# Kernel tuning notes

Measured on AMD Instinct MI355X. Metric: run time of the kernel, lower is better.

The kernel has to match this reference:

```python
import jax, jax.numpy as jnp
import numpy as np

B, S, D, H, M = 2, 2048, 1024, 16, 4096  # batch, seqlen, dim, n_heads, max_seq_len
HD = D // H  # head_dim = 64
EPS = 1e-5


def layernorm(x, g, b):
    mu = jnp.mean(x, axis=-1, keepdims=True)
    var = jnp.mean((x - mu) ** 2, axis=-1, keepdims=True)
    return (x - mu) * jax.lax.rsqrt(var + EPS) * g + b


def setup_inputs() -> dict:
    key = jax.random.key(0)
    ks = jax.random.split(key, 5)
    x = jax.random.normal(ks[0], (B, S, D), jnp.float32)
    # causal mask: >=0 -> keep, negative -> drop (forward does att *= mask >= 0)
    i = jnp.arange(S)
    mask = jnp.where(i[None, :] <= i[:, None], 0, -1).astype(jnp.int32)[None, None]
    w1 = jax.random.normal(ks[1], (4 * D, D), jnp.float32) * (D ** -0.5)
    b1 = jnp.zeros((4 * D,), jnp.float32)
    w2 = jax.random.normal(ks[2], (D, D), jnp.float32) * (D ** -0.5)
    b2 = jnp.zeros((D,), jnp.float32)
    g1 = jnp.ones((D,), jnp.float32)
    beta1 = jnp.zeros((D,), jnp.float32)
    g2 = jnp.ones((D,), jnp.float32)
    beta2 = jnp.zeros((D,), jnp.float32)
    pos_w = jax.random.normal(ks[3], (2 * M - 1,), jnp.float32) * 0.02
    return dict(x=x, mask=mask, w1=w1, b1=b1, w2=w2, b2=b2,
                g1=g1, beta1=beta1, g2=g2, beta2=beta2, pos_w=pos_w)


def reference(x, mask, w1, b1, w2, b2, g1, beta1, g2, beta2, pos_w):
    # f1 + silu, split into gate u and q/k/v
    h = jax.nn.silu(x @ w1.T + b1)                      # [B,S,4D]
    u, q, k, v = jnp.split(h, 4, axis=-1)
    to_heads = lambda t: t.reshape(B, S, H, HD).transpose(0, 2, 1, 3)  # [B,H,S,HD]
    u, q, k, v = map(to_heads, (u, q, k, v))
    # relative positional bias: bias[i,j] = pos_w[M-1 + (j - i)]
    rel = jnp.arange(S)[None, :] - jnp.arange(S)[:, None]
    bias = pos_w[M - 1 + rel]                           # [S,S]
    att = jax.nn.silu(jnp.einsum('bhqd,bhkd->bhqk', q, k) + bias)
    att = att * (mask >= 0)                             # [B,H,S,S]
    y = jnp.einsum('bhqk,bhkd->bhqd', att, v) * u
    y = y.transpose(0, 2, 1, 3).reshape(B, S, D)
    y = layernorm(y, g1, beta1)
    y = y @ w2.T + b2
    return layernorm(y + x, g2, beta2)
```

## Files before the change

kernel.cpp:

```cpp
#include <hip/hip_runtime.h>
#include <hip/hip_bf16.h>

#define BN   2
#define SEQ  2048
#define DIM  1024
#define NH   16
#define HD   64
#define D4   4096
#define MAXS 4096

using bf16 = __hip_bfloat16;
typedef __bf16 bf16x8 __attribute__((ext_vector_type(8)));
typedef float  f32x4  __attribute__((ext_vector_type(4)));

__device__ __forceinline__ float bf2f(bf16 v){ return __bfloat162float(v); }
__device__ __forceinline__ bf16  f2bf(float v){ return __float2bfloat16(v); }
__device__ __forceinline__ float silu_f(float v){
  const float e = __expf(-v);
  return v * __builtin_amdgcn_rcpf(1.f + e);
}

__device__ __forceinline__ void async16(void* lds, const void* g){
  __builtin_amdgcn_global_load_lds((const __attribute__((address_space(1))) void*)g,
                                   (__attribute__((address_space(3))) void*)lds, 16, 0, 0);
}
__device__ __forceinline__ f32x4 mfma16(bf16x8 a, bf16x8 b, f32x4 c){
  return __builtin_amdgcn_mfma_f32_16x16x32_bf16(a, b, c, 0, 0, 0);
}

__global__ __launch_bounds__(256) void f2bk3(
    const float* __restrict__ a, bf16* __restrict__ ao, int na,
    const float* __restrict__ b, bf16* __restrict__ bo, int nb,
    const float* __restrict__ c, bf16* __restrict__ co)
{
  int i = (blockIdx.x * 256 + threadIdx.x) * 4;
  const float* in; bf16* out;
  if (i < na){ in = a; out = ao; }
  else if (i < na + nb){ in = b; out = bo; i -= na; }
  else { in = c; out = co; i -= na + nb; }
  const float4 v = *(const float4*)(in + i);
  bf16 t0 = f2bf(v.x), t1 = f2bf(v.y), t2 = f2bf(v.z), t3 = f2bf(v.w);
  ushort4 o;
  o.x = *(unsigned short*)&t0; o.y = *(unsigned short*)&t1;
  o.z = *(unsigned short*)&t2; o.w = *(unsigned short*)&t3;
  *(ushort4*)((unsigned short*)out + i) = o;
}

template<int NTOT>
__global__ __launch_bounds__(256) void gemm_bt(
    const bf16* __restrict__ A, const bf16* __restrict__ W,
    const float* __restrict__ bias, bf16* __restrict__ outb, bf16* __restrict__ vt)
{
  constexpr int K = DIM;
  const int ntiles = NTOT / 128;
  const int m0 = (int)(blockIdx.x / ntiles) * 128;
  const int n0 = (int)(blockIdx.x % ntiles) * 128;
  __shared__ bf16 Al[2*128*32];
  __shared__ bf16 Bl[2*128*32];
  const int tid = threadIdx.x, wave = tid>>6, lane = tid&63;
  const int quad = lane>>4, l16 = lane&15;
  const int srow = lane>>2;
  const int sg   = ((lane&3) ^ ((lane>>3)&3)) * 8;
  const int wm = (wave>>1)*64, wn = (wave&1)*64;
  const int rkey = ((l16>>1)&3);

  f32x4 acc[4][4];
  #pragma unroll
  for (int i=0;i<4;i++)
    #pragma unroll
    for (int j=0;j<4;j++) acc[i][j] = (f32x4){0.f,0.f,0.f,0.f};

  const bf16* aB = A + m0*K;
  const bf16* wB = W + n0*K;

  for (int k0 = 0; k0 < K; k0 += 64){
    #pragma unroll
    for (int s=0;s<2;s++){
      const int kc = k0 + s*32;
      async16(&Al[s*4096 + wave*1024      ], aB + (wave*32      + srow)*K + kc + sg);
      async16(&Al[s*4096 + wave*1024 + 512], aB + (wave*32 + 16 + srow)*K + kc + sg);
      async16(&Bl[s*4096 + wave*1024      ], wB + (wave*32      + srow)*K + kc + sg);
      async16(&Bl[s*4096 + wave*1024 + 512], wB + (wave*32 + 16 + srow)*K + kc + sg);
    }
    __syncthreads();
    #pragma unroll
    for (int s=0;s<2;s++){
      bf16x8 af[4], bv[4];
      #pragma unroll
      for (int mt=0;mt<4;mt++) af[mt] = *(const bf16x8*)&Al[s*4096 + (wm+mt*16+l16)*32 + (quad ^ rkey)*8];
      #pragma unroll
      for (int nt=0;nt<4;nt++) bv[nt] = *(const bf16x8*)&Bl[s*4096 + (wn+nt*16+l16)*32 + (quad ^ rkey)*8];
      #pragma unroll
      for (int mt=0;mt<4;mt++)
        #pragma unroll
        for (int nt=0;nt<4;nt++)
          acc[mt][nt] = mfma16(af[mt], bv[nt], acc[mt][nt]);
    }
    __syncthreads();
  }

  const bool vtile = (NTOT == 4096) && (n0 >= 3*DIM);
  if (!vtile){
    #pragma unroll
    for (int mt=0;mt<4;mt++){
      #pragma unroll
      for (int nt=0;nt<4;nt++){
        const int row = m0 + wm + mt*16 + quad*4;
        const int col = n0 + wn + nt*16 + l16;
        const float bvv = bias[col];
        #pragma unroll
        for (int r=0;r<4;r++){
          float v = silu_f(acc[mt][nt][r] + bvv);
          outb[(row+r)*NTOT + col] = f2bf(v);
        }
      }
    }
  } else {
    #pragma unroll
    for (int mt=0;mt<4;mt++){
      #pragma unroll
      for (int nt=0;nt<4;nt++){
        const int row = m0 + wm + mt*16 + quad*4;
        const int colg = n0 + wn + nt*16 + l16;
        const float bvv = bias[colg];
        const int col = colg - 3*DIM;
        const int hh = col >> 6, d = col & 63;
        const int bb = row >> 11, sl = row & 2047;
        ushort4 o;
        float v0 = silu_f(acc[mt][nt][0] + bvv);
        float v1 = silu_f(acc[mt][nt][1] + bvv);
        float v2 = silu_f(acc[mt][nt][2] + bvv);
        float v3 = silu_f(acc[mt][nt][3] + bvv);
        bf16 t0=f2bf(v0), t1=f2bf(v1), t2=f2bf(v2), t3=f2bf(v3);
        o.x=*(unsigned short*)&t0; o.y=*(unsigned short*)&t1;
        o.z=*(unsigned short*)&t2; o.w=*(unsigned short*)&t3;
        *(ushort4*)&vt[((bb*NH + hh)*HD + d)*SEQ + sl] = o;
      }
    }
  }
}

__global__ __launch_bounds__(256) void gemm_bt2(
    const bf16* __restrict__ A, const bf16* __restrict__ W,
    const float* __restrict__ bias, const float* __restrict__ resid,
    float* __restrict__ outf)
{
  constexpr int K = DIM, NTOT = DIM;
  const int ntiles = NTOT / 64;
  const int m0 = (int)(blockIdx.x / ntiles) * 128;
  const int n0 = (int)(blockIdx.x % ntiles) * 64;
  __shared__ bf16 Al[2*128*32];
  __shared__ bf16 Bl[2*64*32];
  const int tid = threadIdx.x, wave = tid>>6, lane = tid&63;
  const int quad = lane>>4, l16 = lane&15;
  const int srow = lane>>2;
  const int sg   = ((lane&3) ^ ((lane>>3)&3)) * 8;
  const int wm = wave*32;
  const int rkey = ((l16>>1)&3);

  f32x4 acc[2][4];
  #pragma unroll
  for (int i=0;i<2;i++)
    #pragma unroll
    for (int j=0;j<4;j++) acc[i][j] = (f32x4){0.f,0.f,0.f,0.f};

  const bf16* aB = A + m0*K;
  const bf16* wB = W + n0*K;

  for (int k0 = 0; k0 < K; k0 += 64){
    #pragma unroll
    for (int s=0;s<2;s++){
      const int kc = k0 + s*32;
      async16(&Al[s*4096 + wave*1024      ], aB + (wave*32      + srow)*K + kc + sg);
      async16(&Al[s*4096 + wave*1024 + 512], aB + (wave*32 + 16 + srow)*K + kc + sg);
      async16(&Bl[s*2048 + wave*512       ], wB + (wave*16      + srow)*K + kc + sg);
    }
    __syncthreads();
    #pragma unroll
    for (int s=0;s<2;s++){
      bf16x8 af[2], bv[4];
      #pragma unroll
      for (int mt=0;mt<2;mt++) af[mt] = *(const bf16x8*)&Al[s*4096 + (wm+mt*16+l16)*32 + (quad ^ rkey)*8];
      #pragma unroll
      for (int nt=0;nt<4;nt++) bv[nt] = *(const bf16x8*)&Bl[s*2048 + (nt*16+l16)*32 + (quad ^ rkey)*8];
      #pragma unroll
      for (int mt=0;mt<2;mt++)
        #pragma unroll
        for (int nt=0;nt<4;nt++)
          acc[mt][nt] = mfma16(af[mt], bv[nt], acc[mt][nt]);
    }
    __syncthreads();
  }

  #pragma unroll
  for (int mt=0;mt<2;mt++){
    #pragma unroll
    for (int nt=0;nt<4;nt++){
      const int row = m0 + wm + mt*16 + quad*4;
      const int col = n0 + nt*16 + l16;
      const float bvv = bias[col];
      #pragma unroll
      for (int r=0;r<4;r++){
        outf[(row+r)*NTOT + col] = acc[mt][nt][r] + bvv + resid[(row+r)*NTOT + col];
      }
    }
  }
}

__global__ __launch_bounds__(256) void attn(
    const bf16* __restrict__ h, const bf16* __restrict__ vt,
    const float* __restrict__ pw, bf16* __restrict__ y)
{
  const int bid = blockIdx.x;
  const int g  = bid & 31;
  const int qt = 31 - (bid >> 5);
  const int hh = g & 15, b = g >> 4;

  __shared__ __align__(16) char smem[16384 + 16384 + 17408 + 1024];
  bf16*  Kl  = (bf16*)smem;
  bf16*  Vl  = (bf16*)(smem + 16384);
  bf16*  Pl  = (bf16*)(smem + 32768);
  float* pwl = (float*)(smem + 50176);

  const int tid = threadIdx.x, wave = tid>>6, lane = tid&63;
  const int quad = lane>>4, l16 = lane&15;

  const bf16* kgb = h + b*SEQ*D4 + 2*DIM + hh*HD;
  const bf16* vgb = vt + (b*NH + hh)*HD*SEQ;
  const int krow8 = lane>>3;
  const int kgo   = ((lane&7) ^ krow8) * 8;
  const int vrow4 = lane>>4;

  const int q0 = qt * 64;

  const bf16* qbase = h + (b*SEQ + q0 + wave*16 + l16)*D4 + DIM + hh*HD;
  bf16x8 qf[2];
  qf[0] = *(const bf16x8*)(qbase + quad*8);
  qf[1] = *(const bf16x8*)(qbase + 32 + quad*8);

  f32x4 oacc[4];
  #pragma unroll
  for (int nt=0;nt<4;nt++) oacc[nt] = (f32x4){0.f,0.f,0.f,0.f};

  const int kmax = q0 + 64;

  bf16x8 kreg[4], vreg[4];
  float pv;
  #pragma unroll
  for (int t=0;t<4;t++)
    kreg[t] = *(const bf16x8*)(kgb + (wave*32 + t*8 + krow8)*D4 + kgo);
  #pragma unroll
  for (int t=0;t<4;t++){
    const int vg = ((lane&15) ^ (t*4 + vrow4)) * 8;
    vreg[t] = *(const bf16x8*)(vgb + (wave*16 + t*4 + vrow4)*SEQ + vg);
  }
  pv = pw[MAXS - 1 - q0 - 63 + tid];

  for (int k0 = 0; k0 < kmax; k0 += 128){
    __syncthreads();
    #pragma unroll
    for (int t=0;t<4;t++)
      *(bf16x8*)&Kl[(wave*32 + t*8)*64 + lane*8] = kreg[t];
    #pragma unroll
    for (int t=0;t<4;t++)
      *(bf16x8*)&Vl[(wave*16 + t*4)*128 + lane*8] = vreg[t];
    pwl[tid] = pv;
    __syncthreads();

    if (k0 + 128 < kmax){
      const int kn = k0 + 128;
      #pragma unroll
      for (int t=0;t<4;t++)
        kreg[t] = *(const bf16x8*)(kgb + (kn + wave*32 + t*8 + krow8)*D4 + kgo);
      #pragma unroll
      for (int t=0;t<4;t++){
        const int vg = ((lane&15) ^ (t*4 + vrow4)) * 8;
        vreg[t] = *(const bf16x8*)(vgb + (wave*16 + t*4 + vrow4)*SEQ + kn + vg);
      }
      pv = pw[MAXS - 1 + kn - q0 - 63 + tid];
    }

    f32x4 sacc[8];
    #pragma unroll
    for (int nt=0;nt<8;nt++) sacc[nt] = (f32x4){0.f,0.f,0.f,0.f};
    __builtin_amdgcn_s_setprio(1);
    #pragma unroll
    for (int ks=0;ks<2;ks++){
      #pragma unroll
      for (int nt=0;nt<8;nt++){
        bf16x8 kf = *(const bf16x8*)&Kl[(nt*16 + l16)*64 + ((ks*4 + quad) ^ (l16&7))*8];
        sacc[nt] = mfma16(kf, qf[ks], sacc[nt]);
      }
    }
    __builtin_amdgcn_s_setprio(0);

    bf16* Plw = Pl + wave*(16*136);
    const int dq = q0 - k0;
    const int qrl = wave*16 + l16;
    if (dq >= 127){
      #pragma unroll
      for (int nt=0;nt<8;nt++){
        const int kb = nt*16 + quad*4;
        ushort4 o; bf16 tb[4];
        #pragma unroll
        for (int r=0;r<4;r++){
          const int d = kb + r - qrl;
          const float bias = pwl[d + 63];
          tb[r] = f2bf(silu_f(sacc[nt][r] + bias));
        }
        o.x=*(unsigned short*)&tb[0]; o.y=*(unsigned short*)&tb[1];
        o.z=*(unsigned short*)&tb[2]; o.w=*(unsigned short*)&tb[3];
        *(ushort4*)&Plw[l16*136 + kb] = o;
      }
    } else {
      #pragma unroll
      for (int nt=0;nt<8;nt++){
        const int kb = nt*16 + quad*4;
        ushort4 o; bf16 tb[4];
        #pragma unroll
        for (int r=0;r<4;r++){
          const int d = kb + r - qrl;
          const float bias = pwl[d + 63];
          const float sv = silu_f(sacc[nt][r] + bias);
          tb[r] = f2bf((d <= dq) ? sv : 0.f);
        }
        o.x=*(unsigned short*)&tb[0]; o.y=*(unsigned short*)&tb[1];
        o.z=*(unsigned short*)&tb[2]; o.w=*(unsigned short*)&tb[3];
        *(ushort4*)&Plw[l16*136 + kb] = o;
      }
    }

    __builtin_amdgcn_s_setprio(1);
    #pragma unroll
    for (int ks=0;ks<4;ks++){
      bf16x8 pf = *(const bf16x8*)&Plw[l16*136 + ks*32 + quad*8];
      #pragma unroll
      for (int nt=0;nt<4;nt++){
        bf16x8 vf = *(const bf16x8*)&Vl[(nt*16 + l16)*128 + ((ks*4 + quad) ^ l16)*8];
        oacc[nt] = mfma16(pf, vf, oacc[nt]);
      }
    }
    __builtin_amdgcn_s_setprio(0);
  }

  const int qrow = q0 + wave*16 + quad*4;
  #pragma unroll
  for (int nt=0;nt<4;nt++){
    const int c = hh*HD + nt*16 + l16;
    #pragma unroll
    for (int r=0;r<4;r++){
      const int srow = b*SEQ + qrow + r;
      const float uu = bf2f(h[srow*D4 + c]);
      y[srow*DIM + c] = f2bf(oacc[nt][r] * uu);
    }
  }
}


template<bool FP32IN, bool FP32OUT>
__global__ __launch_bounds__(256) void lnorm(const void* __restrict__ in,
    const float* __restrict__ g, const float* __restrict__ be, void* __restrict__ out)
{
  const int row = blockIdx.x;
  const int tid = threadIdx.x, wave = tid>>6, lane = tid&63;
  const int c0 = tid*4;
  float v[4];
  if (FP32IN){
    const float* p = (const float*)in + row*DIM + c0;
    #pragma unroll
    for (int j=0;j<4;j++) v[j] = p[j];
  } else {
    const bf16* p = (const bf16*)in + row*DIM + c0;
    #pragma unroll
    for (int j=0;j<4;j++) v[j] = bf2f(p[j]);
  }
  float s = 0.f, ss = 0.f;
  #pragma unroll
  for (int j=0;j<4;j++){ s += v[j]; ss += v[j]*v[j]; }
  #pragma unroll
  for (int off=32; off>0; off>>=1){
    s  += __shfl_down(s, off);
    ss += __shfl_down(ss, off);
  }
  __shared__ float red[8];
  if (lane==0){ red[wave] = s; red[4+wave] = ss; }
  __syncthreads();
  s  = red[0]+red[1]+red[2]+red[3];
  ss = red[4]+red[5]+red[6]+red[7];
  const float mu   = s * (1.f/DIM);
  const float var  = ss * (1.f/DIM) - mu*mu;
  const float rstd = rsqrtf(var + 1e-5f);
  #pragma unroll
  for (int j=0;j<4;j++){
    const int c = c0 + j;
    const float o = (v[j]-mu)*rstd*g[c] + be[c];
    if (FP32OUT) ((float*)out)[row*DIM + c] = o;
    else         ((bf16*)out)[row*DIM + c] = f2bf(o);
  }
}

extern "C" void kernel_launch(void* const* d_in, const int* in_sizes, int n_in,
                              void* d_out, int out_size, void* d_ws, size_t ws_size,
                              hipStream_t stream)
{
  const float* x   = (const float*)d_in[0];
  const float* w1  = (const float*)d_in[2];
  const float* b1  = (const float*)d_in[3];
  const float* w2  = (const float*)d_in[4];
  const float* b2  = (const float*)d_in[5];
  const float* g1  = (const float*)d_in[6];
  const float* be1 = (const float*)d_in[7];
  const float* g2  = (const float*)d_in[8];
  const float* be2 = (const float*)d_in[9];
  const float* pw  = (const float*)d_in[10];

  char* ws = (char*)d_ws;
  bf16*  h   = (bf16*)(ws);
  bf16*  vt  = (bf16*)(ws + (32u<<20));
  bf16*  y   = (bf16*)(ws + (40u<<20));
  bf16*  xb  = (bf16*)(ws + (48u<<20));
  bf16*  w1b = (bf16*)(ws + (56u<<20));
  bf16*  w2b = (bf16*)(ws + (64u<<20));
  bf16*  l1  = (bf16*)(ws + (66u<<20));
  float* z   = (float*)(ws + (74u<<20));

  const int NX  = BN*SEQ*DIM;
  const int NW1 = 4*DIM*DIM;
  const int NW2 = DIM*DIM;
  f2bk3<<<dim3((NX+NW1+NW2)/1024), dim3(256), 0, stream>>>(x, xb, NX, w1, w1b, NW1, w2, w2b);

  gemm_bt<4096><<<dim3(1024), dim3(256), 0, stream>>>(xb, w1b, b1, h, vt);
  attn<<<dim3(1024), dim3(256), 0, stream>>>(h, vt, pw, y);
  lnorm<false,false><<<dim3(4096), dim3(256), 0, stream>>>(y, g1, be1, l1);
  gemm_bt2<<<dim3(512), dim3(256), 0, stream>>>(l1, w2b, b2, x, z);
  lnorm<true,true><<<dim3(4096), dim3(256), 0, stream>>>(z, g2, be2, d_out);
}
```

Before: 236.0 us.

## Double-buffer LDS prefetch in both GEMM kernels to overlap loads with MFMA

Both bf16 GEMM kernels now load the first K=32 slice up front. Each loop iteration then issues async global-to-LDS loads for the next slice into the other buffer before running MFMAs on the current one. Before, each iteration loaded two slices, waited at a barrier and only then computed. The goal is to hide global load latency behind matrix math; the barrier count stays the same but each iteration does less work per barrier.

```diff
diff --git a/kernel.cpp b/kernel.cpp
--- a/kernel.cpp
+++ b/kernel.cpp
@@ -52,6 +52,7 @@
     const float* __restrict__ bias, bf16* __restrict__ outb, bf16* __restrict__ vt)
 {
   constexpr int K = DIM;
+  constexpr int NIT = K / 32;
   const int ntiles = NTOT / 128;
   const int m0 = (int)(blockIdx.x / ntiles) * 128;
   const int n0 = (int)(blockIdx.x % ntiles) * 128;
@@ -73,23 +74,31 @@
   const bf16* aB = A + m0*K;
   const bf16* wB = W + n0*K;
 
-  for (int k0 = 0; k0 < K; k0 += 64){
-    #pragma unroll
-    for (int s=0;s<2;s++){
-      const int kc = k0 + s*32;
-      async16(&Al[s*4096 + wave*1024      ], aB + (wave*32      + srow)*K + kc + sg);
-      async16(&Al[s*4096 + wave*1024 + 512], aB + (wave*32 + 16 + srow)*K + kc + sg);
-      async16(&Bl[s*4096 + wave*1024      ], wB + (wave*32      + srow)*K + kc + sg);
-      async16(&Bl[s*4096 + wave*1024 + 512], wB + (wave*32 + 16 + srow)*K + kc + sg);
-    }
-    __syncthreads();
-    #pragma unroll
-    for (int s=0;s<2;s++){
+  {
+    async16(&Al[wave*1024      ], aB + (wave*32      + srow)*K + sg);
+    async16(&Al[wave*1024 + 512], aB + (wave*32 + 16 + srow)*K + sg);
+    async16(&Bl[wave*1024      ], wB + (wave*32      + srow)*K + sg);
+    async16(&Bl[wave*1024 + 512], wB + (wave*32 + 16 + srow)*K + sg);
+  }
+  __syncthreads();
+
+  int cur = 0;
+  for (int it = 0; it < NIT; ++it){
+    if (it + 1 < NIT){
+      const int kc = (it+1)*32;
+      const int nb = (cur^1)*4096;
+      async16(&Al[nb + wave*1024      ], aB + (wave*32      + srow)*K + kc + sg);
+      async16(&Al[nb + wave*1024 + 512], aB + (wave*32 + 16 + srow)*K + kc + sg);
+      async16(&Bl[nb + wave*1024      ], wB + (wave*32      + srow)*K + kc + sg);
+      async16(&Bl[nb + wave*1024 + 512], wB + (wave*32 + 16 + srow)*K + kc + sg);
+    }
+    {
+      const int cb = cur*4096;
       bf16x8 af[4], bv[4];
       #pragma unroll
-      for (int mt=0;mt<4;mt++) af[mt] = *(const bf16x8*)&Al[s*4096 + (wm+mt*16+l16)*32 + (quad ^ rkey)*8];
-      #pragma unroll
-      for (int nt=0;nt<4;nt++) bv[nt] = *(const bf16x8*)&Bl[s*4096 + (wn+nt*16+l16)*32 + (quad ^ rkey)*8];
+      for (int mt=0;mt<4;mt++) af[mt] = *(const bf16x8*)&Al[cb + (wm+mt*16+l16)*32 + (quad ^ rkey)*8];
+      #pragma unroll
+      for (int nt=0;nt<4;nt++) bv[nt] = *(const bf16x8*)&Bl[cb + (wn+nt*16+l16)*32 + (quad ^ rkey)*8];
       #pragma unroll
       for (int mt=0;mt<4;mt++)
         #pragma unroll
@@ -97,6 +106,7 @@
           acc[mt][nt] = mfma16(af[mt], bv[nt], acc[mt][nt]);
     }
     __syncthreads();
+    cur ^= 1;
   }
 
   const bool vtile = (NTOT == 4096) && (n0 >= 3*DIM);
@@ -146,6 +156,7 @@
     float* __restrict__ outf)
 {
   constexpr int K = DIM, NTOT = DIM;
+  constexpr int NIT = K / 32;
   const int ntiles = NTOT / 64;
   const int m0 = (int)(blockIdx.x / ntiles) * 128;
   const int n0 = (int)(blockIdx.x % ntiles) * 64;
@@ -167,22 +178,27 @@
   const bf16* aB = A + m0*K;
   const bf16* wB = W + n0*K;
 
-  for (int k0 = 0; k0 < K; k0 += 64){
-    #pragma unroll
-    for (int s=0;s<2;s++){
-      const int kc = k0 + s*32;
-      async16(&Al[s*4096 + wave*1024      ], aB + (wave*32      + srow)*K + kc + sg);
-      async16(&Al[s*4096 + wave*1024 + 512], aB + (wave*32 + 16 + srow)*K + kc + sg);
-      async16(&Bl[s*2048 + wave*512       ], wB + (wave*16      + srow)*K + kc + sg);
-    }
-    __syncthreads();
-    #pragma unroll
-    for (int s=0;s<2;s++){
+  {
+    async16(&Al[wave*1024      ], aB + (wave*32      + srow)*K + sg);
+    async16(&Al[wave*1024 + 512], aB + (wave*32 + 16 + srow)*K + sg);
+    async16(&Bl[wave*512       ], wB + (wave*16      + srow)*K + sg);
+  }
+  __syncthreads();
+
+  int cur = 0;
+  for (int it = 0; it < NIT; ++it){
+    if (it + 1 < NIT){
+      const int kc = (it+1)*32;
+      async16(&Al[(cur^1)*4096 + wave*1024      ], aB + (wave*32      + srow)*K + kc + sg);
+      async16(&Al[(cur^1)*4096 + wave*1024 + 512], aB + (wave*32 + 16 + srow)*K + kc + sg);
+      async16(&Bl[(cur^1)*2048 + wave*512       ], wB + (wave*16      + srow)*K + kc + sg);
+    }
+    {
       bf16x8 af[2], bv[4];
       #pragma unroll
-      for (int mt=0;mt<2;mt++) af[mt] = *(const bf16x8*)&Al[s*4096 + (wm+mt*16+l16)*32 + (quad ^ rkey)*8];
-      #pragma unroll
-      for (int nt=0;nt<4;nt++) bv[nt] = *(const bf16x8*)&Bl[s*2048 + (nt*16+l16)*32 + (quad ^ rkey)*8];
+      for (int mt=0;mt<2;mt++) af[mt] = *(const bf16x8*)&Al[cur*4096 + (wm+mt*16+l16)*32 + (quad ^ rkey)*8];
+      #pragma unroll
+      for (int nt=0;nt<4;nt++) bv[nt] = *(const bf16x8*)&Bl[cur*2048 + (nt*16+l16)*32 + (quad ^ rkey)*8];
       #pragma unroll
       for (int mt=0;mt<2;mt++)
         #pragma unroll
@@ -190,6 +206,7 @@
           acc[mt][nt] = mfma16(af[mt], bv[nt], acc[mt][nt]);
     }
     __syncthreads();
+    cur ^= 1;
   }
 
   #pragma unroll
```

Measured after the change: 253.7 us. +7.5%, slower.
